# Kernel tuning notes

Hardware: AMD Instinct MI355X
Metric: run time of the kernel (lower is better)

## Reference

```python
import jax, jax.numpy as jnp
import numpy as np

EPS = 1e-7
ROUTINGS = 3

def squash(s, axis=-1):
    # s: capsule vectors; squash along `axis`
    n2 = jnp.sum(s * s, axis=axis, keepdims=True)
    return (n2 / (1.0 + n2) / jnp.sqrt(n2 + EPS)) * s


def setup_inputs() -> dict:
    key = jax.random.key(0)
    k1, k2 = jax.random.split(key)
    B, N, O, Do, Di = 64, 1152, 32, 16, 8
    x = jax.random.normal(k1, (B, N, Di), dtype=jnp.float32)
    weight = 0.01 * jax.random.normal(k2, (N, O, Do, Di), dtype=jnp.float32)
    return {"x": x, "weight": weight}


def reference(x, weight):
    # x: [B, N, Di]; weight: [N, O, Do, Di]
    # x_hat[b,n,o,:] = weight[n,o] @ x[b,n]  -> [B, N, O, Do]
    x_hat = jnp.einsum('noij,bnj->bnoi', weight, x)
    x_hat_det = jax.lax.stop_gradient(x_hat)
    B, N, O, Do = x_hat.shape
    b = jnp.zeros((B, N, O), dtype=x_hat.dtype)
    vj = None
    for i in range(ROUTINGS):
        c = jax.nn.softmax(b, axis=2)  # [B, N, O] over output capsules
        xh = x_hat if i == ROUTINGS - 1 else x_hat_det
        s = jnp.einsum('bno,bnoi->boi', c, xh)  # sum over input capsules
        vj = squash(s, axis=-1)  # [B, O, Do]
        if i < ROUTINGS - 1:
            # agreement: <x_hat[b,n,o], vj[b,o]>
            b = b + jnp.einsum('bnoi,boi->bno', x_hat_det, vj)
    return vj  # [B, O, Do]
```

## Files before the change

### kernel.cpp

```cpp
#include <hip/hip_runtime.h>

#define Bb 64
#define Nn 1152
#define Oo 32
#define DOv 16
#define DIv 8
#define BPB 32
#define NG 4

__device__ __forceinline__ void gload_lds16(const void* g, void* l) {
    __builtin_amdgcn_global_load_lds(
        (const __attribute__((address_space(1))) unsigned*)g,
        (__attribute__((address_space(3))) unsigned*)l, 16, 0, 0);
}

__global__ __launch_bounds__(256) void caps_route(
    const float* __restrict__ x,
    const float* __restrict__ w,
    const float* __restrict__ vcum,
    float* __restrict__ spart,
    int nc)
{
    const int t  = threadIdx.x;
    const int o  = t & 31;
    const int bl = t >> 5;
    const int n0 = blockIdx.x * nc;
    const int b0 = blockIdx.y * BPB;

    __shared__ float4 wbuf[2][1024];
    __shared__ float4 xbuf[16][BPB][2];

    int gq[4];
#pragma unroll
    for (int k = 0; k < 4; ++k) {
        int p = k * 256 + t;
        gq[k] = (p & ~31) | ((p ^ (p >> 5)) & 31);
    }

    auto stageW = [&](int n, int c) {
        const float4* wg = (const float4*)(w + (size_t)n * (Oo * DOv * DIv));
#pragma unroll
        for (int k = 0; k < 4; ++k)
            gload_lds16(&wg[gq[k]], &wbuf[c][k * 256 + t]);
    };
    auto stageX = [&](int nb) {
        int cnt = min(16, nc - nb);
        for (int q = t; q < cnt * BPB * 2; q += 256) {
            int nn = q >> 6, bb = (q >> 1) & 31, h = q & 1;
            xbuf[nn][bb][h] = ((const float4*)(
                x + ((size_t)(b0 + bb) * Nn + (size_t)(n0 + nb + nn)) * DIv))[h];
        }
    };

    const bool have_v = (vcum != nullptr);
    float vc[NG][DOv];
    if (have_v) {
#pragma unroll
        for (int g = 0; g < NG; ++g)
#pragma unroll
            for (int i = 0; i < DOv; ++i)
                vc[g][i] = vcum[((size_t)(b0 + 8 * g + bl) * Oo + o) * DOv + i];
    }

    float sacc[NG][DOv];
#pragma unroll
    for (int g = 0; g < NG; ++g)
#pragma unroll
        for (int i = 0; i < DOv; ++i) sacc[g][i] = 0.f;

    stageX(0);
    stageW(n0, 0);
    int cur = 0;

    for (int nn = 0; nn < nc; ++nn) {
        if (nn && (nn & 15) == 0) { __syncthreads(); stageX(nn); }
        __syncthreads();
        if (nn + 1 < nc) stageW(n0 + nn + 1, cur ^ 1);

        float xa[NG][DIv];
#pragma unroll
        for (int g = 0; g < NG; ++g) {
            float4 v0 = xbuf[nn & 15][8 * g + bl][0];
            float4 v1 = xbuf[nn & 15][8 * g + bl][1];
            xa[g][0] = v0.x; xa[g][1] = v0.y; xa[g][2] = v0.z; xa[g][3] = v0.w;
            xa[g][4] = v1.x; xa[g][5] = v1.y; xa[g][6] = v1.z; xa[g][7] = v1.w;
        }

        float xh[NG][DOv];
#pragma unroll
        for (int g = 0; g < NG; ++g)
#pragma unroll
            for (int i = 0; i < DOv; ++i) xh[g][i] = 0.f;

#pragma unroll
        for (int i2 = 0; i2 < 32; ++i2) {
            float4 wv = wbuf[cur][o * 32 + (i2 ^ o)];
            const int i = i2 >> 1, jb = (i2 & 1) * 4;
#pragma unroll
            for (int g = 0; g < NG; ++g) {
                xh[g][i] = fmaf(wv.x, xa[g][jb + 0], xh[g][i]);
                xh[g][i] = fmaf(wv.y, xa[g][jb + 1], xh[g][i]);
                xh[g][i] = fmaf(wv.z, xa[g][jb + 2], xh[g][i]);
                xh[g][i] = fmaf(wv.w, xa[g][jb + 3], xh[g][i]);
            }
        }

        float c[NG];
        if (have_v) {
            float e[NG], ssum[NG];
#pragma unroll
            for (int g = 0; g < NG; ++g) {
                float l = 0.f;
#pragma unroll
                for (int i = 0; i < DOv; ++i) l += xh[g][i] * vc[g][i];
                e[g] = __expf(l);
                ssum[g] = e[g];
            }
#pragma unroll
            for (int d = 16; d >= 1; d >>= 1)
#pragma unroll
                for (int g = 0; g < NG; ++g)
                    ssum[g] += __shfl_xor(ssum[g], d);
#pragma unroll
            for (int g = 0; g < NG; ++g) c[g] = e[g] / ssum[g];
        } else {
#pragma unroll
            for (int g = 0; g < NG; ++g) c[g] = 1.0f / 32.0f;
        }

#pragma unroll
        for (int g = 0; g < NG; ++g)
#pragma unroll
            for (int i = 0; i < DOv; ++i) sacc[g][i] += c[g] * xh[g][i];
        cur ^= 1;
    }

    float* p = spart + (size_t)blockIdx.x * (Bb * Oo * DOv);
#pragma unroll
    for (int g = 0; g < NG; ++g) {
        float* pg = p + ((size_t)(b0 + 8 * g + bl) * Oo + o) * DOv;
#pragma unroll
        for (int i = 0; i < DOv; ++i) pg[i] = sacc[g][i];
    }
}

__global__ __launch_bounds__(64) void caps_squash(
    const float* __restrict__ spart, int nch,
    const float* __restrict__ vin,
    float* __restrict__ vout,
    float* __restrict__ out)
{
    const int b = blockIdx.x, oo = blockIdx.y;
    const int t = threadIdx.x;
    const int i = t & 15, pg = t >> 4;
    const size_t base = ((size_t)b * Oo + oo) * DOv + i;
    float s = 0.f;
#pragma unroll 4
    for (int p = pg; p < nch; p += 4)
        s += spart[(size_t)p * (Bb * Oo * DOv) + base];
    s += __shfl_xor(s, 16);
    s += __shfl_xor(s, 32);
    float n2 = s * s;
#pragma unroll
    for (int d = 8; d >= 1; d >>= 1) n2 += __shfl_xor(n2, d);
    float vj = s * (n2 / ((1.f + n2) * sqrtf(n2 + 1e-7f)));
    if (t < 16) {
        if (vout) vout[base] = (vin ? vin[base] : 0.f) + vj;
        if (out)  out[base]  = vj;
    }
}

extern "C" void kernel_launch(void* const* d_in, const int* in_sizes, int n_in,
                              void* d_out, int out_size, void* d_ws, size_t ws_size,
                              hipStream_t stream)
{
    const float* x = (const float*)d_in[0];
    const float* w = (const float*)d_in[1];
    float* out = (float*)d_out;

    static const int cfgs[][2] = {{128,9},{72,16},{36,32},{18,64},{9,128},{4,288},{2,576},{1,1152}};
    int nch = 1, nc = 1152;
    for (auto& c : cfgs) {
        size_t need = ((size_t)c[0] * Bb * Oo * DOv + (size_t)Bb * Oo * DOv) * sizeof(float);
        if (need <= ws_size) { nch = c[0]; nc = c[1]; break; }
    }

    float* spart = (float*)d_ws;
    float* vcum  = spart + (size_t)nch * Bb * Oo * DOv;

    dim3 grid(nch, Bb / BPB), blk(256);
    dim3 sgrid(Bb, Oo), sblk(64);

    caps_route<<<grid, blk, 0, stream>>>(x, w, nullptr, spart, nc);
    caps_squash<<<sgrid, sblk, 0, stream>>>(spart, nch, nullptr, vcum, nullptr);
    caps_route<<<grid, blk, 0, stream>>>(x, w, vcum, spart, nc);
    caps_squash<<<sgrid, sblk, 0, stream>>>(spart, nch, vcum, vcum, nullptr);
    caps_route<<<grid, blk, 0, stream>>>(x, w, vcum, spart, nc);
    caps_squash<<<sgrid, sblk, 0, stream>>>(spart, nch, nullptr, nullptr, out);
}
```

Measured before the change: 103.7 us.

## Restructure capsule routing: split Do across lanes, stage two capsules, finer N-split

The routing kernel now splits the 16 output dims across two half-warps, so each thread handles 8 batch rows for 8 dims. Two input capsules' weights are staged per double-buffered step, which halves the barriers. x and vcum are read directly from global memory instead of being staged in LDS, and launch bounds request two blocks per CU. The N dimension is split into more chunks (up to 288) for more parallelism, and the squash kernel is vectorized with float4 to cover the larger partial count. The cost is more partial-sum traffic and extra cross-lane shuffles for the softmax.

```diff
diff --git a/kernel.cpp b/kernel.cpp
--- a/kernel.cpp
+++ b/kernel.cpp
@@ -6,7 +6,7 @@
 #define DOv 16
 #define DIv 8
 #define BPB 32
-#define NG 4
+#define NG 8
 
 __device__ __forceinline__ void gload_lds16(const void* g, void* l) {
     __builtin_amdgcn_global_load_lds(
@@ -14,7 +14,7 @@
         (__attribute__((address_space(3))) unsigned*)l, 16, 0, 0);
 }
 
-__global__ __launch_bounds__(256) void caps_route(
+__global__ __launch_bounds__(256, 2) void caps_route(
     const float* __restrict__ x,
     const float* __restrict__ w,
     const float* __restrict__ vcum,
@@ -23,12 +23,12 @@
 {
     const int t  = threadIdx.x;
     const int o  = t & 31;
-    const int bl = t >> 5;
+    const int ih = (t >> 5) & 1;
+    const int wv = __builtin_amdgcn_readfirstlane(t >> 6);
     const int n0 = blockIdx.x * nc;
-    const int b0 = blockIdx.y * BPB;
-
-    __shared__ float4 wbuf[2][1024];
-    __shared__ float4 xbuf[16][BPB][2];
+    const int b0 = blockIdx.y * BPB + wv * NG;
+
+    __shared__ float4 wbuf[2][2][1024];
 
     int gq[4];
 #pragma unroll
@@ -36,111 +36,113 @@
         int p = k * 256 + t;
         gq[k] = (p & ~31) | ((p ^ (p >> 5)) & 31);
     }
-
-    auto stageW = [&](int n, int c) {
-        const float4* wg = (const float4*)(w + (size_t)n * (Oo * DOv * DIv));
-#pragma unroll
-        for (int k = 0; k < 4; ++k)
-            gload_lds16(&wg[gq[k]], &wbuf[c][k * 256 + t]);
-    };
-    auto stageX = [&](int nb) {
-        int cnt = min(16, nc - nb);
-        for (int q = t; q < cnt * BPB * 2; q += 256) {
-            int nn = q >> 6, bb = (q >> 1) & 31, h = q & 1;
-            xbuf[nn][bb][h] = ((const float4*)(
-                x + ((size_t)(b0 + bb) * Nn + (size_t)(n0 + nb + nn)) * DIv))[h];
+    auto stageW2 = [&](int n, int c) {
+#pragma unroll
+        for (int s2 = 0; s2 < 2; ++s2) {
+            const float4* wg = (const float4*)(w + (size_t)(n + s2) * (Oo * DOv * DIv));
+#pragma unroll
+            for (int k = 0; k < 4; ++k)
+                gload_lds16(&wg[gq[k]], &wbuf[c][s2][k * 256 + t]);
         }
     };
 
     const bool have_v = (vcum != nullptr);
-    float vc[NG][DOv];
-    if (have_v) {
-#pragma unroll
-        for (int g = 0; g < NG; ++g)
-#pragma unroll
-            for (int i = 0; i < DOv; ++i)
-                vc[g][i] = vcum[((size_t)(b0 + 8 * g + bl) * Oo + o) * DOv + i];
-    }
-
-    float sacc[NG][DOv];
+    float sacc[NG][8];
 #pragma unroll
     for (int g = 0; g < NG; ++g)
 #pragma unroll
-        for (int i = 0; i < DOv; ++i) sacc[g][i] = 0.f;
-
-    stageX(0);
-    stageW(n0, 0);
+        for (int i = 0; i < 8; ++i) sacc[g][i] = 0.f;
+
+    stageW2(n0, 0);
+    __syncthreads();
     int cur = 0;
 
-    for (int nn = 0; nn < nc; ++nn) {
-        if (nn && (nn & 15) == 0) { __syncthreads(); stageX(nn); }
+    for (int pp = 0; pp < (nc >> 1); ++pp) {
+        if (pp + 1 < (nc >> 1)) stageW2(n0 + 2 * pp + 2, cur ^ 1);
+
+#pragma unroll
+        for (int s2 = 0; s2 < 2; ++s2) {
+            const int n = n0 + 2 * pp + s2;
+
+            float xs[NG][DIv];
+#pragma unroll
+            for (int g = 0; g < NG; ++g) {
+                const float* xp = x + ((size_t)(b0 + g) * Nn + n) * DIv;
+#pragma unroll
+                for (int j = 0; j < DIv; ++j) xs[g][j] = xp[j];
+            }
+
+            float xh[NG][8];
+#pragma unroll
+            for (int g = 0; g < NG; ++g)
+#pragma unroll
+                for (int i = 0; i < 8; ++i) xh[g][i] = 0.f;
+#pragma unroll
+            for (int k = 0; k < 16; ++k) {
+                const int i2 = ih * 16 + k;
+                float4 wv4 = wbuf[cur][s2][o * 32 + ((i2 ^ o) & 31)];
+                const int ii = k >> 1, jb = (k & 1) * 4;
+#pragma unroll
+                for (int g = 0; g < NG; ++g) {
+                    xh[g][ii] = fmaf(wv4.x, xs[g][jb + 0], xh[g][ii]);
+                    xh[g][ii] = fmaf(wv4.y, xs[g][jb + 1], xh[g][ii]);
+                    xh[g][ii] = fmaf(wv4.z, xs[g][jb + 2], xh[g][ii]);
+                    xh[g][ii] = fmaf(wv4.w, xs[g][jb + 3], xh[g][ii]);
+                }
+            }
+
+            float c[NG];
+            if (have_v) {
+                float l[NG];
+#pragma unroll
+                for (int g = 0; g < NG; ++g) {
+                    const float* vp = vcum + (((size_t)(b0 + g) * Oo + o) * DOv + ih * 8);
+                    float4 v0 = ((const float4*)vp)[0], v1 = ((const float4*)vp)[1];
+                    float lp = xh[g][0] * v0.x + xh[g][1] * v0.y + xh[g][2] * v0.z + xh[g][3] * v0.w
+                             + xh[g][4] * v1.x + xh[g][5] * v1.y + xh[g][6] * v1.z + xh[g][7] * v1.w;
+                    l[g] = lp + __shfl_xor(lp, 32);
+                }
+                float e[NG];
+#pragma unroll
+                for (int g = 0; g < NG; ++g) e[g] = __expf(l[g]);
+
+                float r[4];
+#pragma unroll
+                for (int k4 = 0; k4 < 4; ++k4) r[k4] = ih ? e[k4 + 4] : e[k4];
+#pragma unroll
+                for (int d = 16; d >= 1; d >>= 1)
+#pragma unroll
+                    for (int k4 = 0; k4 < 4; ++k4) r[k4] += __shfl_xor(r[k4], d);
+                float ro[4];
+#pragma unroll
+                for (int k4 = 0; k4 < 4; ++k4) ro[k4] = __shfl_xor(r[k4], 32);
+#pragma unroll
+                for (int k4 = 0; k4 < 4; ++k4) {
+                    float slo = ih ? ro[k4] : r[k4];
+                    float shi = ih ? r[k4] : ro[k4];
+                    c[k4]     = e[k4]     * __builtin_amdgcn_rcpf(slo);
+                    c[k4 + 4] = e[k4 + 4] * __builtin_amdgcn_rcpf(shi);
+                }
+            } else {
+#pragma unroll
+                for (int g = 0; g < NG; ++g) c[g] = 1.0f / 32.0f;
+            }
+
+#pragma unroll
+            for (int g = 0; g < NG; ++g)
+#pragma unroll
+                for (int i = 0; i < 8; ++i) sacc[g][i] += c[g] * xh[g][i];
+        }
         __syncthreads();
-        if (nn + 1 < nc) stageW(n0 + nn + 1, cur ^ 1);
-
-        float xa[NG][DIv];
-#pragma unroll
-        for (int g = 0; g < NG; ++g) {
-            float4 v0 = xbuf[nn & 15][8 * g + bl][0];
-            float4 v1 = xbuf[nn & 15][8 * g + bl][1];
-            xa[g][0] = v0.x; xa[g][1] = v0.y; xa[g][2] = v0.z; xa[g][3] = v0.w;
-            xa[g][4] = v1.x; xa[g][5] = v1.y; xa[g][6] = v1.z; xa[g][7] = v1.w;
-        }
-
-        float xh[NG][DOv];
-#pragma unroll
-        for (int g = 0; g < NG; ++g)
-#pragma unroll
-            for (int i = 0; i < DOv; ++i) xh[g][i] = 0.f;
-
-#pragma unroll
-        for (int i2 = 0; i2 < 32; ++i2) {
-            float4 wv = wbuf[cur][o * 32 + (i2 ^ o)];
-            const int i = i2 >> 1, jb = (i2 & 1) * 4;
-#pragma unroll
-            for (int g = 0; g < NG; ++g) {
-                xh[g][i] = fmaf(wv.x, xa[g][jb + 0], xh[g][i]);
-                xh[g][i] = fmaf(wv.y, xa[g][jb + 1], xh[g][i]);
-                xh[g][i] = fmaf(wv.z, xa[g][jb + 2], xh[g][i]);
-                xh[g][i] = fmaf(wv.w, xa[g][jb + 3], xh[g][i]);
-            }
-        }
-
-        float c[NG];
-        if (have_v) {
-            float e[NG], ssum[NG];
-#pragma unroll
-            for (int g = 0; g < NG; ++g) {
-                float l = 0.f;
-#pragma unroll
-                for (int i = 0; i < DOv; ++i) l += xh[g][i] * vc[g][i];
-                e[g] = __expf(l);
-                ssum[g] = e[g];
-            }
-#pragma unroll
-            for (int d = 16; d >= 1; d >>= 1)
-#pragma unroll
-                for (int g = 0; g < NG; ++g)
-                    ssum[g] += __shfl_xor(ssum[g], d);
-#pragma unroll
-            for (int g = 0; g < NG; ++g) c[g] = e[g] / ssum[g];
-        } else {
-#pragma unroll
-            for (int g = 0; g < NG; ++g) c[g] = 1.0f / 32.0f;
-        }
-
-#pragma unroll
-        for (int g = 0; g < NG; ++g)
-#pragma unroll
-            for (int i = 0; i < DOv; ++i) sacc[g][i] += c[g] * xh[g][i];
         cur ^= 1;
     }
 
     float* p = spart + (size_t)blockIdx.x * (Bb * Oo * DOv);
 #pragma unroll
     for (int g = 0; g < NG; ++g) {
-        float* pg = p + ((size_t)(b0 + 8 * g + bl) * Oo + o) * DOv;
-#pragma unroll
-        for (int i = 0; i < DOv; ++i) pg[i] = sacc[g][i];
+        float* pg = p + (((size_t)(b0 + g) * Oo + o) * DOv + ih * 8);
+        ((float4*)pg)[0] = make_float4(sacc[g][0], sacc[g][1], sacc[g][2], sacc[g][3]);
+        ((float4*)pg)[1] = make_float4(sacc[g][4], sacc[g][5], sacc[g][6], sacc[g][7]);
     }
 }
 
@@ -152,21 +154,33 @@
 {
     const int b = blockIdx.x, oo = blockIdx.y;
     const int t = threadIdx.x;
-    const int i = t & 15, pg = t >> 4;
-    const size_t base = ((size_t)b * Oo + oo) * DOv + i;
-    float s = 0.f;
-#pragma unroll 4
-    for (int p = pg; p < nch; p += 4)
-        s += spart[(size_t)p * (Bb * Oo * DOv) + base];
-    s += __shfl_xor(s, 16);
-    s += __shfl_xor(s, 32);
-    float n2 = s * s;
-#pragma unroll
-    for (int d = 8; d >= 1; d >>= 1) n2 += __shfl_xor(n2, d);
-    float vj = s * (n2 / ((1.f + n2) * sqrtf(n2 + 1e-7f)));
-    if (t < 16) {
-        if (vout) vout[base] = (vin ? vin[base] : 0.f) + vj;
-        if (out)  out[base]  = vj;
+    const int q = t & 3, pg = t >> 2;
+    const size_t base4 = ((size_t)b * Oo + oo) * (DOv / 4) + q;
+    const float4* sp4 = (const float4*)spart;
+    const size_t chunk4 = (size_t)Bb * Oo * DOv / 4;
+
+    float4 s = make_float4(0.f, 0.f, 0.f, 0.f);
+    for (int p = pg; p < nch; p += 16) {
+        float4 v = sp4[(size_t)p * chunk4 + base4];
+        s.x += v.x; s.y += v.y; s.z += v.z; s.w += v.w;
+    }
+#pragma unroll
+    for (int d = 4; d <= 32; d <<= 1) {
+        s.x += __shfl_xor(s.x, d); s.y += __shfl_xor(s.y, d);
+        s.z += __shfl_xor(s.z, d); s.w += __shfl_xor(s.w, d);
+    }
+    float n2 = s.x * s.x + s.y * s.y + s.z * s.z + s.w * s.w;
+    n2 += __shfl_xor(n2, 1);
+    n2 += __shfl_xor(n2, 2);
+    float sc = n2 / ((1.f + n2) * sqrtf(n2 + 1e-7f));
+    if (t < 4) {
+        float4 vj = make_float4(s.x * sc, s.y * sc, s.z * sc, s.w * sc);
+        size_t i4 = base4;
+        if (vout) {
+            float4 vi = vin ? ((const float4*)vin)[i4] : make_float4(0.f, 0.f, 0.f, 0.f);
+            ((float4*)vout)[i4] = make_float4(vi.x + vj.x, vi.y + vj.y, vi.z + vj.z, vi.w + vj.w);
+        }
+        if (out) ((float4*)out)[i4] = vj;
     }
 }
 
@@ -178,8 +192,8 @@
     const float* w = (const float*)d_in[1];
     float* out = (float*)d_out;
 
-    static const int cfgs[][2] = {{128,9},{72,16},{36,32},{18,64},{9,128},{4,288},{2,576},{1,1152}};
-    int nch = 1, nc = 1152;
+    static const int cfgs[][2] = {{288,4},{144,8},{72,16},{36,32},{18,64},{8,144},{4,288},{2,576}};
+    int nch = 2, nc = 576;
     for (auto& c : cfgs) {
         size_t need = ((size_t)c[0] * Bb * Oo * DOv + (size_t)Bb * Oo * DOv) * sizeof(float);
         if (need <= ws_size) { nch = c[0]; nc = c[1]; break; }
```

Measured after the change: 185.5 us. +78.8%, slower.
